# Optimization experiments

Hardware: AMD Instinct MI355X
Metric: run time of the kernel (lower is better)

Reference implementation:

```python
import jax, jax.numpy as jnp
import numpy as np


def _forward(hidden_states, edge_src, edge_tgt, edge_label, gcn_W, gcn_b,
             attn_w, attn_b, ms_W1, ms_b1, ms_w2, ms_b2, ant_w, ant_b, span_width):
    B, S, H = hidden_states.shape
    L = gcn_W.shape[0]
    # ---- GCNLayer: per-label linear on gathered source nodes, scatter-add to targets
    src = edge_src.reshape(-1)
    tgt = edge_tgt.reshape(-1)
    lab = edge_label.reshape(-1)
    E = edge_src.shape[1]
    bidx = jnp.repeat(jnp.arange(B), E)                      # [Et]
    src_emb = hidden_states[bidx, src]                       # [Et, H]
    transformed = jnp.zeros_like(src_emb)
    for l in range(L):                                       # fixed small label set
        y = src_emb @ gcn_W[l].T + gcn_b[l]
        transformed = jnp.where((lab == l)[:, None], y, transformed)
    valid = (lab != -100) & (src < S) & (tgt < S)
    transformed = jnp.where(valid[:, None], transformed, 0.0)
    flat = bidx * S + tgt
    gcn_out = jnp.zeros((B * S, H), hidden_states.dtype).at[flat].add(transformed)
    gcn_out = jax.nn.relu(gcn_out.reshape(B, S, H))
    embeddings = hidden_states + gcn_out                     # combine_strategy='add'
    # ---- candidate spans: all (i, j), j in [i, min(i+W, S)), static per S
    Wsp = int(span_width)
    i = np.arange(S)[:, None]
    w = np.arange(Wsp)[None, :]
    ok = (i + w) < S
    starts = np.broadcast_to(i, (S, Wsp))[ok]                # [Nsp]
    ends = (i + w)[ok]                                       # [Nsp]
    tok_idx_np = starts[:, None] + np.arange(Wsp)[None, :]   # [Nsp, Wsp]
    tok_mask = jnp.asarray(tok_idx_np <= ends[:, None])
    tok_idx = jnp.asarray(np.minimum(tok_idx_np, S - 1))
    # ---- SpanRepresentation: [start_emb ; end_emb ; attention-pooled]
    span_tok = embeddings[:, tok_idx]                        # [B, Nsp, Wsp, H]
    scores = jnp.einsum('bnwh,h->bnw', span_tok, attn_w) + attn_b[0]
    scores = jnp.where(tok_mask[None], scores, -1e30)
    attn = jax.nn.softmax(scores, axis=-1)                   # softmax over span tokens
    pooled = jnp.einsum('bnw,bnwh->bnh', attn, span_tok)
    span_reps = jnp.concatenate(
        [embeddings[:, jnp.asarray(starts)], embeddings[:, jnp.asarray(ends)], pooled],
        axis=-1)                                             # [B, Nsp, 3H]
    # ---- MentionScorer: Linear -> ReLU -> Linear(.,1)
    hdn = jax.nn.relu(jnp.einsum('bnd,ed->bne', span_reps, ms_W1) + ms_b1)
    mention = jnp.einsum('bne,e->bn', hdn, ms_w2) + ms_b2[0]  # [B, Nsp]
    # ---- prune: k = int(0.4 * seq_len); attention_mask is all ones -> static
    k = int(0.4 * S)
    _, top_idx = jax.lax.top_k(mention, k)
    pruned = jnp.take_along_axis(span_reps, top_idx[..., None], axis=1)  # [B, k, 3H]
    # ---- antecedent scorer: Linear on cat([reps_j, reps_i]) decomposes into two dots
    D = span_reps.shape[-1]
    s_j = pruned @ ant_w[:D]                                 # weight on first (column) slot
    s_i = pruned @ ant_w[D:]                                 # weight on second (row) slot
    ant = s_j[:, None, :] + s_i[:, :, None] + ant_b[0]       # [B, k, k]; ant[b,i,j]
    ant = jnp.concatenate([jnp.zeros((B, k, 1), ant.dtype), ant], axis=-1)
    tri = jnp.triu(jnp.ones((k, k), bool), 0)                # mask j >= i
    mext = jnp.concatenate([jnp.zeros((k, 1), bool), tri], axis=1)
    masked = jnp.where(mext[None], jnp.asarray(-1e10, ant.dtype), ant)
    return jnp.log(jax.nn.softmax(masked, axis=-1) + 1e-10)  # [B, k, k+1]


def setup_inputs() -> dict:
    key = jax.random.key(0)
    ks = jax.random.split(key, 10)
    B, S, H, L, E, W = 2, 256, 768, 50, 512, 10
    return {
        'hidden_states': jax.random.normal(ks[0], (B, S, H), jnp.float32),
        'attention_mask': jnp.ones((B, S), jnp.int32),
        'edge_src': jax.random.randint(ks[1], (B, E), 0, S),
        'edge_tgt': jax.random.randint(ks[2], (B, E), 0, S),
        'edge_label': jax.random.randint(ks[3], (B, E), 0, L),
        'gcn_W': jax.random.normal(ks[4], (L, H, H), jnp.float32) * 0.02,
        'gcn_b': jnp.zeros((L, H), jnp.float32),
        'attn_w': jax.random.normal(ks[5], (H,), jnp.float32) * 0.02,
        'attn_b': jnp.zeros((1,), jnp.float32),
        'ms_W1': jax.random.normal(ks[6], (3 * H, 3 * H), jnp.float32) * 0.02,
        'ms_b1': jnp.zeros((3 * H,), jnp.float32),
        'ms_w2': jax.random.normal(ks[7], (3 * H,), jnp.float32) * 0.02,
        'ms_b2': jnp.zeros((1,), jnp.float32),
        'ant_w': jax.random.normal(ks[8], (6 * H,), jnp.float32) * 0.02,
        'ant_b': jnp.zeros((1,), jnp.float32),
        'span_width': 10,
    }


def reference(hidden_states, attention_mask, edge_src, edge_tgt, edge_label,
              gcn_W, gcn_b, attn_w, attn_b, ms_W1, ms_b1, ms_w2, ms_b2,
              ant_w, ant_b, span_width):
    del attention_mask  # all ones; seq_len == S, so k = int(0.4 * S) is static
    return _forward(hidden_states, edge_src, edge_tgt, edge_label, gcn_W, gcn_b,
                    attn_w, attn_b, ms_W1, ms_b1, ms_w2, ms_b2, ant_w, ant_b, span_width)
```

## Files before the change

### kernel.cpp

```cpp
#include <hip/hip_runtime.h>
#include <math.h>

#define B 2
#define S 256
#define H 768
#define L 50
#define E 512
#define W 10
#define NSPAN 2515
#define KTOP 102
#define D3 2304
#define N6 6912

#define OFF_GOUT ((size_t)0)
#define OFF_EMB  ((size_t)393216)
#define OFF_G    ((size_t)786432)
#define OFF_TOKD ((size_t)4325376)
#define OFF_MENT ((size_t)4329472)
#define OFF_SJ   ((size_t)4334592)
#define OFF_SI   ((size_t)4339712)
#define OFF_SELJ ((size_t)4344832)
#define OFF_SELI ((size_t)4345088)
#define OFF_INT  ((size_t)4345344)

__global__ __launch_bounds__(1024) void k_group(
    const int* __restrict__ esrc, const int* __restrict__ etgt,
    const int* __restrict__ elab, int* __restrict__ cnt,
    int* __restrict__ off, int* __restrict__ edges) {
    __shared__ int lcnt[L];
    __shared__ int loff[L];
    int t = threadIdx.x;
    if (t < L) lcnt[t] = 0;
    __syncthreads();
    int lab = elab[t], src = esrc[t], tgt = etgt[t];
    bool valid = (lab >= 0) && (lab < L) && (src >= 0) && (src < S) && (tgt >= 0) && (tgt < S);
    int mypos = -1;
    if (valid) mypos = atomicAdd(&lcnt[lab], 1);
    __syncthreads();
    if (t == 0) {
        int acc = 0;
        for (int l = 0; l < L; l++) { loff[l] = acc; acc += lcnt[l]; }
    }
    __syncthreads();
    if (valid) edges[loff[lab] + mypos] = t;
    if (t < L) { cnt[t] = lcnt[t]; off[t] = loff[t]; }
}

#define GK 384
__global__ __launch_bounds__(256) void k_gcn(
    const float* __restrict__ hidden, const float* __restrict__ gcnW,
    const float* __restrict__ gcnb, const int* __restrict__ cnt,
    const int* __restrict__ off, const int* __restrict__ edges,
    const int* __restrict__ esrc, const int* __restrict__ etgt,
    float* __restrict__ gout) {
    int l = blockIdx.y;
    int n = cnt[l];
    if (n == 0) return;
    int row0 = blockIdx.x * 64;
    int kbase = blockIdx.z * GK;
    __shared__ float Ws[32][68];
    __shared__ float Xs[32][34];
    __shared__ int srow[32];
    __shared__ int trow[32];
    int tid = threadIdx.x;
    int tx = tid & 15, ty = tid >> 4;
    int o = off[l];
    for (int e0 = 0; e0 < n; e0 += 32) {
        int nv = min(32, n - e0);
        if (tid < 32) {
            int sr = 0, tr = 0;
            if (tid < nv) {
                int g = edges[o + e0 + tid];
                int bb = g / E;
                sr = (bb * S + esrc[g]) * H;
                tr = (bb * S + etgt[g]) * H;
            }
            srow[tid] = sr;
            trow[tid] = tr;
        }
        __syncthreads();
        float acc[4][2];
#pragma unroll
        for (int r = 0; r < 4; r++) { acc[r][0] = 0.f; acc[r][1] = 0.f; }
        for (int kc = 0; kc < GK; kc += 32) {
            int k0 = kbase + kc;
#pragma unroll
            for (int j = 0; j < 2; j++) {
                int f = tid + 256 * j;
                int r = f >> 3, kq = (f & 7) * 4;
                float4 v = *(const float4*)(gcnW + ((size_t)l * H + row0 + r) * H + k0 + kq);
                Ws[kq + 0][r] = v.x; Ws[kq + 1][r] = v.y;
                Ws[kq + 2][r] = v.z; Ws[kq + 3][r] = v.w;
            }
#pragma unroll
            for (int j = 0; j < 4; j++) {
                int f = tid + 256 * j;
                int e = f >> 5, kk = f & 31;
                Xs[kk][e] = hidden[srow[e] + k0 + kk];
            }
            __syncthreads();
#pragma unroll
            for (int k = 0; k < 32; k++) {
                float4 a = *(const float4*)&Ws[k][ty * 4];
                float2 x2 = *(const float2*)&Xs[k][tx * 2];
                acc[0][0] = fmaf(a.x, x2.x, acc[0][0]);
                acc[1][0] = fmaf(a.y, x2.x, acc[1][0]);
                acc[2][0] = fmaf(a.z, x2.x, acc[2][0]);
                acc[3][0] = fmaf(a.w, x2.x, acc[3][0]);
                acc[0][1] = fmaf(a.x, x2.y, acc[0][1]);
                acc[1][1] = fmaf(a.y, x2.y, acc[1][1]);
                acc[2][1] = fmaf(a.z, x2.y, acc[2][1]);
                acc[3][1] = fmaf(a.w, x2.y, acc[3][1]);
            }
            __syncthreads();
        }
        const float* bp = gcnb + l * H + row0 + ty * 4;
        bool addb = (blockIdx.z == 0);
#pragma unroll
        for (int e = 0; e < 2; e++) {
            int ei = tx * 2 + e;
            if (ei < nv) {
                int base = trow[ei] + row0 + ty * 4;
#pragma unroll
                for (int r = 0; r < 4; r++) {
                    float v = acc[r][e];
                    if (addb) v += bp[r];
                    atomicAdd(&gout[base + r], v);
                }
            }
        }
        __syncthreads();
    }
}

__global__ __launch_bounds__(256) void k_embdots(
    const float* __restrict__ hidden, const float* __restrict__ gout,
    const float* __restrict__ attnw, const float* __restrict__ antw,
    float* __restrict__ emb, float* __restrict__ tokd) {
    int wave = threadIdx.x >> 6, lane = threadIdx.x & 63;
    int tok = blockIdx.x * 4 + wave;
    const float* hp = hidden + (size_t)tok * H;
    const float* gp = gout + (size_t)tok * H;
    float* ep = emb + (size_t)tok * H;
    float p[7] = {0, 0, 0, 0, 0, 0, 0};
#pragma unroll
    for (int m = 0; m < 12; m++) {
        int k = lane + 64 * m;
        float e = hp[k] + fmaxf(gp[k], 0.f);
        ep[k] = e;
        p[0] = fmaf(attnw[k], e, p[0]);
#pragma unroll
        for (int q = 0; q < 6; q++) p[1 + q] = fmaf(antw[q * H + k], e, p[1 + q]);
    }
#pragma unroll
    for (int q = 0; q < 7; q++) {
        float v = p[q];
#pragma unroll
        for (int d = 32; d; d >>= 1) v += __shfl_down(v, d);
        p[q] = v;
    }
    if (lane == 0) {
        float* o = tokd + (size_t)tok * 8;
#pragma unroll
        for (int q = 0; q < 7; q++) o[q] = p[q];
    }
}

__global__ __launch_bounds__(256) void k_gemm(
    const float* __restrict__ A, const float* __restrict__ W1, float* __restrict__ G) {
    __shared__ float As[32][68];
    __shared__ float Bs[32][132];
    int n0 = blockIdx.x * 128;
    int m0 = blockIdx.y * 64;
    int blk = n0 / D3;
    int e0 = n0 - blk * D3;
    const float* Ap = A + (size_t)m0 * H;
    const float* Bp = W1 + (size_t)e0 * D3 + blk * H;
    int tid = threadIdx.x;
    int tx = tid & 15, ty = tid >> 4;
    float4 pa[2], pb[4];
#pragma unroll
    for (int j = 0; j < 2; j++) {
        int f = tid + 256 * j;
        pa[j] = *(const float4*)(Ap + (size_t)(f >> 3) * H + (f & 7) * 4);
    }
#pragma unroll
    for (int j = 0; j < 4; j++) {
        int f = tid + 256 * j;
        pb[j] = *(const float4*)(Bp + (size_t)(f >> 3) * D3 + (f & 7) * 4);
    }
    float acc[4][8];
#pragma unroll
    for (int r = 0; r < 4; r++)
#pragma unroll
        for (int c = 0; c < 8; c++) acc[r][c] = 0.f;
    for (int kt = 0; kt < H; kt += 32) {
#pragma unroll
        for (int j = 0; j < 2; j++) {
            int f = tid + 256 * j;
            int row = f >> 3, c4 = (f & 7) * 4;
            As[c4 + 0][row] = pa[j].x; As[c4 + 1][row] = pa[j].y;
            As[c4 + 2][row] = pa[j].z; As[c4 + 3][row] = pa[j].w;
        }
#pragma unroll
        for (int j = 0; j < 4; j++) {
            int f = tid + 256 * j;
            int row = f >> 3, c4 = (f & 7) * 4;
            Bs[c4 + 0][row] = pb[j].x; Bs[c4 + 1][row] = pb[j].y;
            Bs[c4 + 2][row] = pb[j].z; Bs[c4 + 3][row] = pb[j].w;
        }
        __syncthreads();
        if (kt + 32 < H) {
            int kn = kt + 32;
#pragma unroll
            for (int j = 0; j < 2; j++) {
                int f = tid + 256 * j;
                pa[j] = *(const float4*)(Ap + (size_t)(f >> 3) * H + kn + (f & 7) * 4);
            }
#pragma unroll
            for (int j = 0; j < 4; j++) {
                int f = tid + 256 * j;
                pb[j] = *(const float4*)(Bp + (size_t)(f >> 3) * D3 + kn + (f & 7) * 4);
            }
        }
#pragma unroll
        for (int k = 0; k < 32; k++) {
            float4 a  = *(const float4*)&As[k][ty * 4];
            float4 b0 = *(const float4*)&Bs[k][tx * 8];
            float4 b1 = *(const float4*)&Bs[k][tx * 8 + 4];
            float av[4] = {a.x, a.y, a.z, a.w};
            float bv[8] = {b0.x, b0.y, b0.z, b0.w, b1.x, b1.y, b1.z, b1.w};
#pragma unroll
            for (int r = 0; r < 4; r++)
#pragma unroll
                for (int c = 0; c < 8; c++) acc[r][c] = fmaf(av[r], bv[c], acc[r][c]);
        }
        __syncthreads();
    }
#pragma unroll
    for (int r = 0; r < 4; r++) {
        float* gp = G + (size_t)(m0 + ty * 4 + r) * N6 + n0 + tx * 8;
        *(float4*)gp       = make_float4(acc[r][0], acc[r][1], acc[r][2], acc[r][3]);
        *(float4*)(gp + 4) = make_float4(acc[r][4], acc[r][5], acc[r][6], acc[r][7]);
    }
}

__global__ __launch_bounds__(256) void k_span(
    const float* __restrict__ G, const float* __restrict__ tokd,
    const float* __restrict__ b1, const float* __restrict__ w2,
    const float* __restrict__ b2, float* __restrict__ ment,
    float* __restrict__ sjA, float* __restrict__ siA) {
    int b = blockIdx.x / S, start = blockIdx.x % S;
    int nw = min(W, S - start);
    int tail = S - start;
    int base = (start <= S - W) ? start * W
             : (S - W + 1) * W + ((W - 1) * W / 2 - tail * (tail + 1) / 2);
    __shared__ float sc[W];
    __shared__ float aw[W][W];
    __shared__ float redA[4][W];
    int tid = threadIdx.x;
    if (tid < nw) sc[tid] = tokd[(size_t)(b * S + start + tid) * 8];
    __syncthreads();
    if (tid < nw) {
        int w = tid;
        float mx = sc[0];
        for (int j = 1; j <= w; j++) mx = fmaxf(mx, sc[j]);
        float sum = 0.f;
        for (int j = 0; j <= w; j++) { float e = expf(sc[j] - mx); aw[w][j] = e; sum += e; }
        float inv = 1.f / sum;
        for (int j = 0; j <= w; j++) aw[w][j] *= inv;
        const float* td = tokd + (size_t)(b * S) * 8;
        float sj = td[start * 8 + 1] + td[(start + w) * 8 + 2];
        float si = td[start * 8 + 4] + td[(start + w) * 8 + 5];
        for (int j = 0; j <= w; j++) {
            sj = fmaf(aw[w][j], td[(start + j) * 8 + 3], sj);
            si = fmaf(aw[w][j], td[(start + j) * 8 + 6], si);
        }
        sjA[b * NSPAN + base + w] = sj;
        siA[b * NSPAN + base + w] = si;
    }
    __syncthreads();
    float mloc[W];
#pragma unroll
    for (int w = 0; w < W; w++) mloc[w] = 0.f;
    const float* Gb = G + (size_t)(b * S) * N6;
    for (int e = tid; e < D3; e += 256) {
        float a = Gb[(size_t)start * N6 + e] + b1[e];
        float w2e = w2[e];
        float cj[W], bm[W];
#pragma unroll
        for (int j = 0; j < W; j++) {
            if (j < nw) {
                cj[j] = Gb[(size_t)(start + j) * N6 + 2 * D3 + e];
                bm[j] = Gb[(size_t)(start + j) * N6 + D3 + e];
            } else { cj[j] = 0.f; bm[j] = 0.f; }
        }
#pragma unroll
        for (int w = 0; w < W; w++) {
            if (w < nw) {
                float pre = a + bm[w];
#pragma unroll
                for (int j = 0; j <= w; j++) pre = fmaf(aw[w][j], cj[j], pre);
                mloc[w] += fmaxf(pre, 0.f) * w2e;
            }
        }
    }
    int wave = tid >> 6, lane = tid & 63;
#pragma unroll
    for (int w = 0; w < W; w++) {
        float v = mloc[w];
#pragma unroll
        for (int d = 32; d; d >>= 1) v += __shfl_down(v, d);
        if (lane == 0) redA[wave][w] = v;
    }
    __syncthreads();
    if (tid < nw)
        ment[b * NSPAN + base + tid] =
            redA[0][tid] + redA[1][tid] + redA[2][tid] + redA[3][tid] + b2[0];
}

__global__ __launch_bounds__(256) void k_topk(
    const float* __restrict__ ment, const float* __restrict__ sjA,
    const float* __restrict__ siA, float* __restrict__ selj, float* __restrict__ seli) {
    __shared__ unsigned int uv[NSPAN];
    __shared__ int hist[256];
    __shared__ int suf[256];
    __shared__ int cand_i[160];
    __shared__ unsigned int cand_u[160];
    __shared__ int ncand;
    __shared__ unsigned int s_prefix;
    __shared__ int s_kk;
    int b = blockIdx.x, tid = threadIdx.x;
    for (int n = tid; n < NSPAN; n += 256) {
        unsigned int u = __float_as_uint(ment[b * NSPAN + n]);
        uv[n] = (u & 0x80000000u) ? ~u : (u | 0x80000000u);
    }
    if (tid == 0) { s_prefix = 0u; s_kk = KTOP; ncand = 0; }
    __syncthreads();
    for (int pass = 3; pass >= 0; pass--) {
        int shift = pass * 8;
        hist[tid] = 0;
        __syncthreads();
        unsigned int pref = s_prefix;
        unsigned int pmask = (pass == 3) ? 0u : (0xFFFFFFFFu << (shift + 8));
        for (int n = tid; n < NSPAN; n += 256) {
            unsigned int u = uv[n];
            if ((u & pmask) == pref) atomicAdd(&hist[(u >> shift) & 255], 1);
        }
        __syncthreads();
        suf[tid] = hist[tid];
        __syncthreads();
        for (int d2 = 1; d2 < 256; d2 <<= 1) {
            int y = suf[tid] + ((tid + d2 < 256) ? suf[tid + d2] : 0);
            __syncthreads();
            suf[tid] = y;
            __syncthreads();
        }
        int kk = s_kk;
        __syncthreads();
        if (suf[tid] >= kk && (tid == 255 || suf[tid + 1] < kk)) {
            s_prefix = pref | ((unsigned int)tid << shift);
            s_kk = kk - ((tid == 255) ? 0 : suf[tid + 1]);
        }
        __syncthreads();
    }
    unsigned int uk = s_prefix;
    for (int n = tid; n < NSPAN; n += 256) {
        if (uv[n] >= uk) {
            int p = atomicAdd(&ncand, 1);
            if (p < 160) { cand_i[p] = n; cand_u[p] = uv[n]; }
        }
    }
    __syncthreads();
    int nc = min(ncand, 160);
    for (int c = tid; c < nc; c += 256) {
        unsigned int u = cand_u[c];
        int idx = cand_i[c];
        int rank = 0;
        for (int d = 0; d < nc; d++) {
            unsigned int ud = cand_u[d];
            if (ud > u || (ud == u && cand_i[d] < idx)) rank++;
        }
        if (rank < KTOP) {
            selj[b * KTOP + rank] = sjA[b * NSPAN + idx];
            seli[b * KTOP + rank] = siA[b * NSPAN + idx];
        }
    }
}

__global__ __launch_bounds__(128) void k_ant(
    const float* __restrict__ selj, const float* __restrict__ seli,
    const float* __restrict__ antb, float* __restrict__ out) {
    int b = blockIdx.x / KTOP, i = blockIdx.x % KTOP;
    int c = threadIdx.x;
    float v = -3.0e38f;
    if (c == 0) v = 0.f;
    else if (c <= KTOP) {
        int j = c - 1;
        v = (j >= i) ? -1e10f : (selj[b * KTOP + j] + seli[b * KTOP + i] + antb[0]);
    }
    __shared__ float r2[2];
    int wave = c >> 6, lane = c & 63;
    float mv = v;
#pragma unroll
    for (int d = 32; d; d >>= 1) mv = fmaxf(mv, __shfl_down(mv, d));
    if (lane == 0) r2[wave] = mv;
    __syncthreads();
    float mx = fmaxf(r2[0], r2[1]);
    __syncthreads();
    float ex = (c <= KTOP) ? expf(v - mx) : 0.f;
    float sv = ex;
#pragma unroll
    for (int d = 32; d; d >>= 1) sv += __shfl_down(sv, d);
    if (lane == 0) r2[wave] = sv;
    __syncthreads();
    float sm = r2[0] + r2[1];
    if (c <= KTOP)
        out[(size_t)(b * KTOP + i) * (KTOP + 1) + c] = logf(ex / sm + 1e-10f);
}

extern "C" void kernel_launch(void* const* d_in, const int* in_sizes, int n_in,
                              void* d_out, int out_size, void* d_ws, size_t ws_size,
                              hipStream_t stream) {
    (void)in_sizes; (void)n_in; (void)out_size; (void)ws_size;
    const float* hidden = (const float*)d_in[0];
    const int*   esrc   = (const int*)d_in[2];
    const int*   etgt   = (const int*)d_in[3];
    const int*   elab   = (const int*)d_in[4];
    const float* gcnW   = (const float*)d_in[5];
    const float* gcnb   = (const float*)d_in[6];
    const float* attnw  = (const float*)d_in[7];
    const float* msW1   = (const float*)d_in[9];
    const float* msb1   = (const float*)d_in[10];
    const float* msw2   = (const float*)d_in[11];
    const float* msb2   = (const float*)d_in[12];
    const float* antw   = (const float*)d_in[13];
    const float* antb   = (const float*)d_in[14];
    float* out = (float*)d_out;

    float* wsf  = (float*)d_ws;
    float* gout = wsf + OFF_GOUT;
    float* emb  = wsf + OFF_EMB;
    float* G    = wsf + OFF_G;
    float* tokd = wsf + OFF_TOKD;
    float* ment = wsf + OFF_MENT;
    float* sjA  = wsf + OFF_SJ;
    float* siA  = wsf + OFF_SI;
    float* selj = wsf + OFF_SELJ;
    float* seli = wsf + OFF_SELI;
    int* wsi   = (int*)(wsf + OFF_INT);
    int* cnt   = wsi;
    int* off   = wsi + 64;
    int* edges = wsi + 128;

    hipMemsetAsync(gout, 0, (size_t)B * S * H * sizeof(float), stream);
    k_group<<<1, B * E, 0, stream>>>(esrc, etgt, elab, cnt, off, edges);
    k_gcn<<<dim3(12, L, 2), 256, 0, stream>>>(hidden, gcnW, gcnb, cnt, off, edges, esrc, etgt, gout);
    k_embdots<<<B * S / 4, 256, 0, stream>>>(hidden, gout, attnw, antw, emb, tokd);
    k_gemm<<<dim3(N6 / 128, B * S / 64), 256, 0, stream>>>(emb, msW1, G);
    k_span<<<B * S, 256, 0, stream>>>(G, tokd, msb1, msw2, msb2, ment, sjA, siA);
    k_topk<<<B, 256, 0, stream>>>(ment, sjA, siA, selj, seli);
    k_ant<<<B * KTOP, 128, 0, stream>>>(selj, seli, antb, out);
}
```

Before: 368.1 us.

## Transpose GEMM operands for vectorized tile loads and split span scoring across blocks

Adds a tiled transpose kernel that writes transposed copies of the mention-scorer weight and the embeddings before the GEMM. The GEMM can then store its A and B tiles to shared memory with float4 writes instead of scattered scalar transposing stores. Separately, k_span now launches one block per 256-wide hidden chunk, span start and batch, and accumulates mention scores with float atomics into a zeroed buffer. This trades extra transpose traffic (the full weight matrix is rewritten on every call) and atomic reductions for higher parallelism. It also drops the b2 bias, which only shifts all mention scores equally.

```diff
diff --git a/kernel.cpp b/kernel.cpp
--- a/kernel.cpp
+++ b/kernel.cpp
@@ -22,6 +22,8 @@
 #define OFF_SELJ ((size_t)4344832)
 #define OFF_SELI ((size_t)4345088)
 #define OFF_INT  ((size_t)4345344)
+#define OFF_EMBT ((size_t)4347392)
+#define OFF_W1T  ((size_t)4740608)
 
 __global__ __launch_bounds__(1024) void k_group(
     const int* __restrict__ esrc, const int* __restrict__ etgt,
@@ -44,6 +46,26 @@
     __syncthreads();
     if (valid) edges[loff[lab] + mypos] = t;
     if (t < L) { cnt[t] = lcnt[t]; off[t] = loff[t]; }
+}
+
+__global__ __launch_bounds__(256) void k_trans(
+    const float* __restrict__ in, float* __restrict__ out, int R, int C) {
+    __shared__ float T[32][33];
+    int c0 = blockIdx.x * 32, r0 = blockIdx.y * 32;
+    int tid = threadIdx.x;
+    int cc = tid & 31, r8 = tid >> 5;
+#pragma unroll
+    for (int i = 0; i < 4; i++) {
+        int rr = r8 + 8 * i;
+        T[rr][cc] = in[(size_t)(r0 + rr) * C + c0 + cc];
+    }
+    __syncthreads();
+    int rr2 = tid & 31, c8 = tid >> 5;
+#pragma unroll
+    for (int i = 0; i < 4; i++) {
+        int cc2 = c8 + 8 * i;
+        out[(size_t)(c0 + cc2) * R + r0 + rr2] = T[rr2][cc2];
+    }
 }
 
 #define GK 384
@@ -167,27 +189,27 @@
 }
 
 __global__ __launch_bounds__(256) void k_gemm(
-    const float* __restrict__ A, const float* __restrict__ W1, float* __restrict__ G) {
+    const float* __restrict__ embT, const float* __restrict__ W1T, float* __restrict__ G) {
     __shared__ float As[32][68];
     __shared__ float Bs[32][132];
     int n0 = blockIdx.x * 128;
     int m0 = blockIdx.y * 64;
     int blk = n0 / D3;
     int e0 = n0 - blk * D3;
-    const float* Ap = A + (size_t)m0 * H;
-    const float* Bp = W1 + (size_t)e0 * D3 + blk * H;
     int tid = threadIdx.x;
     int tx = tid & 15, ty = tid >> 4;
+    const float* Ap = embT + m0;
+    const float* Bp = W1T + (size_t)(blk * H) * D3 + e0;
     float4 pa[2], pb[4];
 #pragma unroll
     for (int j = 0; j < 2; j++) {
         int f = tid + 256 * j;
-        pa[j] = *(const float4*)(Ap + (size_t)(f >> 3) * H + (f & 7) * 4);
+        pa[j] = *(const float4*)(Ap + (size_t)(f >> 4) * 512 + (f & 15) * 4);
     }
 #pragma unroll
     for (int j = 0; j < 4; j++) {
         int f = tid + 256 * j;
-        pb[j] = *(const float4*)(Bp + (size_t)(f >> 3) * D3 + (f & 7) * 4);
+        pb[j] = *(const float4*)(Bp + (size_t)(f >> 5) * D3 + (f & 31) * 4);
     }
     float acc[4][8];
 #pragma unroll
@@ -198,16 +220,12 @@
 #pragma unroll
         for (int j = 0; j < 2; j++) {
             int f = tid + 256 * j;
-            int row = f >> 3, c4 = (f & 7) * 4;
-            As[c4 + 0][row] = pa[j].x; As[c4 + 1][row] = pa[j].y;
-            As[c4 + 2][row] = pa[j].z; As[c4 + 3][row] = pa[j].w;
+            *(float4*)&As[f >> 4][(f & 15) * 4] = pa[j];
         }
 #pragma unroll
         for (int j = 0; j < 4; j++) {
             int f = tid + 256 * j;
-            int row = f >> 3, c4 = (f & 7) * 4;
-            Bs[c4 + 0][row] = pb[j].x; Bs[c4 + 1][row] = pb[j].y;
-            Bs[c4 + 2][row] = pb[j].z; Bs[c4 + 3][row] = pb[j].w;
+            *(float4*)&Bs[f >> 5][(f & 31) * 4] = pb[j];
         }
         __syncthreads();
         if (kt + 32 < H) {
@@ -215,19 +233,19 @@
 #pragma unroll
             for (int j = 0; j < 2; j++) {
                 int f = tid + 256 * j;
-                pa[j] = *(const float4*)(Ap + (size_t)(f >> 3) * H + kn + (f & 7) * 4);
+                pa[j] = *(const float4*)(Ap + (size_t)(kn + (f >> 4)) * 512 + (f & 15) * 4);
             }
 #pragma unroll
             for (int j = 0; j < 4; j++) {
                 int f = tid + 256 * j;
-                pb[j] = *(const float4*)(Bp + (size_t)(f >> 3) * D3 + kn + (f & 7) * 4);
+                pb[j] = *(const float4*)(Bp + (size_t)(kn + (f >> 5)) * D3 + (f & 31) * 4);
             }
         }
 #pragma unroll
         for (int k = 0; k < 32; k++) {
             float4 a  = *(const float4*)&As[k][ty * 4];
-            float4 b0 = *(const float4*)&Bs[k][tx * 8];
-            float4 b1 = *(const float4*)&Bs[k][tx * 8 + 4];
+            float4 b0 = *(const float4*)&Bs[k][tx * 4];
+            float4 b1 = *(const float4*)&Bs[k][tx * 4 + 64];
             float av[4] = {a.x, a.y, a.z, a.w};
             float bv[8] = {b0.x, b0.y, b0.z, b0.w, b1.x, b1.y, b1.z, b1.w};
 #pragma unroll
@@ -239,84 +257,73 @@
     }
 #pragma unroll
     for (int r = 0; r < 4; r++) {
-        float* gp = G + (size_t)(m0 + ty * 4 + r) * N6 + n0 + tx * 8;
-        *(float4*)gp       = make_float4(acc[r][0], acc[r][1], acc[r][2], acc[r][3]);
-        *(float4*)(gp + 4) = make_float4(acc[r][4], acc[r][5], acc[r][6], acc[r][7]);
+        float* gp = G + (size_t)(m0 + ty * 4 + r) * N6 + n0;
+        *(float4*)(gp + tx * 4)      = make_float4(acc[r][0], acc[r][1], acc[r][2], acc[r][3]);
+        *(float4*)(gp + tx * 4 + 64) = make_float4(acc[r][4], acc[r][5], acc[r][6], acc[r][7]);
     }
 }
 
 __global__ __launch_bounds__(256) void k_span(
     const float* __restrict__ G, const float* __restrict__ tokd,
     const float* __restrict__ b1, const float* __restrict__ w2,
-    const float* __restrict__ b2, float* __restrict__ ment,
-    float* __restrict__ sjA, float* __restrict__ siA) {
-    int b = blockIdx.x / S, start = blockIdx.x % S;
+    float* __restrict__ ment, float* __restrict__ sjA, float* __restrict__ siA) {
+    int ec = blockIdx.x;
+    int start = blockIdx.y;
+    int b = blockIdx.z;
     int nw = min(W, S - start);
     int tail = S - start;
     int base = (start <= S - W) ? start * W
              : (S - W + 1) * W + ((W - 1) * W / 2 - tail * (tail + 1) / 2);
-    __shared__ float sc[W];
-    __shared__ float aw[W][W];
-    __shared__ float redA[4][W];
+    __shared__ float aw[W][W + 1];
     int tid = threadIdx.x;
-    if (tid < nw) sc[tid] = tokd[(size_t)(b * S + start + tid) * 8];
-    __syncthreads();
+    const float* td = tokd + (size_t)(b * S) * 8;
     if (tid < nw) {
         int w = tid;
-        float mx = sc[0];
-        for (int j = 1; j <= w; j++) mx = fmaxf(mx, sc[j]);
+        float sc[W];
+        float mx = -3.0e38f;
+        for (int j = 0; j <= w; j++) { sc[j] = td[(start + j) * 8]; mx = fmaxf(mx, sc[j]); }
         float sum = 0.f;
         for (int j = 0; j <= w; j++) { float e = expf(sc[j] - mx); aw[w][j] = e; sum += e; }
         float inv = 1.f / sum;
         for (int j = 0; j <= w; j++) aw[w][j] *= inv;
-        const float* td = tokd + (size_t)(b * S) * 8;
-        float sj = td[start * 8 + 1] + td[(start + w) * 8 + 2];
-        float si = td[start * 8 + 4] + td[(start + w) * 8 + 5];
-        for (int j = 0; j <= w; j++) {
-            sj = fmaf(aw[w][j], td[(start + j) * 8 + 3], sj);
-            si = fmaf(aw[w][j], td[(start + j) * 8 + 6], si);
-        }
-        sjA[b * NSPAN + base + w] = sj;
-        siA[b * NSPAN + base + w] = si;
-    }
-    __syncthreads();
-    float mloc[W];
-#pragma unroll
-    for (int w = 0; w < W; w++) mloc[w] = 0.f;
+        if (ec == 0) {
+            float sj = td[start * 8 + 1] + td[(start + w) * 8 + 2];
+            float si = td[start * 8 + 4] + td[(start + w) * 8 + 5];
+            for (int j = 0; j <= w; j++) {
+                sj = fmaf(aw[w][j], td[(start + j) * 8 + 3], sj);
+                si = fmaf(aw[w][j], td[(start + j) * 8 + 6], si);
+            }
+            sjA[b * NSPAN + base + w] = sj;
+            siA[b * NSPAN + base + w] = si;
+        }
+    }
+    __syncthreads();
+    int e = ec * 256 + tid;
     const float* Gb = G + (size_t)(b * S) * N6;
-    for (int e = tid; e < D3; e += 256) {
-        float a = Gb[(size_t)start * N6 + e] + b1[e];
-        float w2e = w2[e];
-        float cj[W], bm[W];
-#pragma unroll
-        for (int j = 0; j < W; j++) {
-            if (j < nw) {
-                cj[j] = Gb[(size_t)(start + j) * N6 + 2 * D3 + e];
-                bm[j] = Gb[(size_t)(start + j) * N6 + D3 + e];
-            } else { cj[j] = 0.f; bm[j] = 0.f; }
-        }
-#pragma unroll
-        for (int w = 0; w < W; w++) {
-            if (w < nw) {
-                float pre = a + bm[w];
-#pragma unroll
-                for (int j = 0; j <= w; j++) pre = fmaf(aw[w][j], cj[j], pre);
-                mloc[w] += fmaxf(pre, 0.f) * w2e;
-            }
-        }
-    }
-    int wave = tid >> 6, lane = tid & 63;
+    float a = Gb[(size_t)start * N6 + e] + b1[e];
+    float w2e = w2[e];
+    float cj[W], bm[W];
+#pragma unroll
+    for (int j = 0; j < W; j++) {
+        if (j < nw) {
+            cj[j] = Gb[(size_t)(start + j) * N6 + 2 * D3 + e];
+            bm[j] = Gb[(size_t)(start + j) * N6 + D3 + e];
+        } else { cj[j] = 0.f; bm[j] = 0.f; }
+    }
+    int lane = tid & 63;
 #pragma unroll
     for (int w = 0; w < W; w++) {
-        float v = mloc[w];
+        float v = 0.f;
+        if (w < nw) {
+            float pre = a + bm[w];
+#pragma unroll
+            for (int j = 0; j <= w; j++) pre = fmaf(aw[w][j], cj[j], pre);
+            v = fmaxf(pre, 0.f) * w2e;
+        }
 #pragma unroll
         for (int d = 32; d; d >>= 1) v += __shfl_down(v, d);
-        if (lane == 0) redA[wave][w] = v;
-    }
-    __syncthreads();
-    if (tid < nw)
-        ment[b * NSPAN + base + tid] =
-            redA[0][tid] + redA[1][tid] + redA[2][tid] + redA[3][tid] + b2[0];
+        if (lane == 0 && w < nw) atomicAdd(&ment[b * NSPAN + base + w], v);
+    }
 }
 
 __global__ __launch_bounds__(256) void k_topk(
@@ -433,7 +440,6 @@
     const float* msW1   = (const float*)d_in[9];
     const float* msb1   = (const float*)d_in[10];
     const float* msw2   = (const float*)d_in[11];
-    const float* msb2   = (const float*)d_in[12];
     const float* antw   = (const float*)d_in[13];
     const float* antb   = (const float*)d_in[14];
     float* out = (float*)d_out;
@@ -448,17 +454,22 @@
     float* siA  = wsf + OFF_SI;
     float* selj = wsf + OFF_SELJ;
     float* seli = wsf + OFF_SELI;
+    float* embT = wsf + OFF_EMBT;
+    float* W1T  = wsf + OFF_W1T;
     int* wsi   = (int*)(wsf + OFF_INT);
     int* cnt   = wsi;
     int* off   = wsi + 64;
     int* edges = wsi + 128;
 
     hipMemsetAsync(gout, 0, (size_t)B * S * H * sizeof(float), stream);
+    hipMemsetAsync(ment, 0, (size_t)B * NSPAN * sizeof(float), stream);
     k_group<<<1, B * E, 0, stream>>>(esrc, etgt, elab, cnt, off, edges);
+    k_trans<<<dim3(D3 / 32, D3 / 32), 256, 0, stream>>>(msW1, W1T, D3, D3);
     k_gcn<<<dim3(12, L, 2), 256, 0, stream>>>(hidden, gcnW, gcnb, cnt, off, edges, esrc, etgt, gout);
     k_embdots<<<B * S / 4, 256, 0, stream>>>(hidden, gout, attnw, antw, emb, tokd);
-    k_gemm<<<dim3(N6 / 128, B * S / 64), 256, 0, stream>>>(emb, msW1, G);
-    k_span<<<B * S, 256, 0, stream>>>(G, tokd, msb1, msw2, msb2, ment, sjA, siA);
+    k_trans<<<dim3(H / 32, (B * S) / 32), 256, 0, stream>>>(emb, embT, B * S, H);
+    k_gemm<<<dim3(N6 / 128, B * S / 64), 256, 0, stream>>>(embT, W1T, G);
+    k_span<<<dim3(D3 / 256, S, B), 256, 0, stream>>>(G, tokd, msb1, msw2, ment, sjA, siA);
     k_topk<<<B, 256, 0, stream>>>(ment, sjA, siA, selj, seli);
     k_ant<<<B * KTOP, 128, 0, stream>>>(selj, seli, antb, out);
 }
```

Result: slower. 450.1 us (+22.3%).
